# Kernel optimization log

Hardware: AMD Instinct MI355X
Metric: run time of the kernel (lower is better)

## Reference

```python
import jax, jax.numpy as jnp
import numpy as np
import math

B, H, L, D = 4, 16, 8192, 64


def setup_inputs() -> dict:
    key = jax.random.key(0)
    kq, kk, kv, kmu = jax.random.split(key, 4)
    Q = jax.random.normal(kq, (B, H, L, D), dtype=jnp.float32)
    K = jax.random.normal(kk, (B, H, L, D), dtype=jnp.float32)
    V = jax.random.normal(kv, (B, H, L, D), dtype=jnp.float32)
    mask = jnp.ones((B, L), dtype=jnp.float32)
    # learned params (multi_gauss=True): pi init [0.5,0.5]; mu ~ N(0,0.5) with mu[0]=0
    pi = jnp.array([0.5, 0.5], dtype=jnp.float32)
    mu = jax.random.normal(kmu, (2, H, D), dtype=jnp.float32) * 0.5
    mu = mu * jnp.array([0.0, 1.0], dtype=jnp.float32)[:, None, None]
    return {"Q": Q, "K": K, "V": V, "mask": mask, "pi": pi, "mu": mu}


def reference(Q, K, V, mask, pi, mu):
    # mixture-of-Gaussian keys: shift K by two learned means, convex-combine
    p = jnp.clip(pi, 0.0, 1.0)
    K1 = K - mu[0][None, :, None, :]
    K2 = K - mu[1][None, :, None, :]
    Km = K1 * p[0] + K2 * p[1]
    # kernelized linear attention: phi(x) = elu(x)+1, scaled by 1/L^0.25
    L_ = Q.shape[2]
    s = 1.0 / math.sqrt(math.sqrt(L_))
    m = mask[:, None, :, None]  # [B,1,L,1]
    Qf = (jax.nn.elu(Q) + 1.0) * s
    Kf = (jax.nn.elu(Km) + 1.0) * m * s
    Vm = V * m
    # K^T V first: [B,H,D,D] state, then Q @ state -> [B,H,L,D]
    KV = jnp.einsum('bhld,bhle->bhde', Kf, Vm)
    return jnp.einsum('bhld,bhde->bhle', Qf, KV)
```

## Files before the change

kernel.cpp:

```cpp
#include <hip/hip_runtime.h>
#include <cstddef>
#include <stdint.h>

#define L_ 8192
#define BH_ 64
#define SCALE 0.1051120519067143f
#define SLD 72

typedef __attribute__((ext_vector_type(8))) short bf16x8;
typedef __attribute__((ext_vector_type(4))) float f32x4;

__device__ __forceinline__ float elu1(float x) {
    return x > 0.0f ? (x + 1.0f) : __expf(x);
}
__device__ __forceinline__ unsigned short f2bf(float x) {
    unsigned u = __float_as_uint(x);
    u += 0x7fffu + ((u >> 16) & 1u);
    return (unsigned short)(u >> 16);
}

__global__ __launch_bounds__(256) void zero_kernel(float4* __restrict__ p) {
    p[(size_t)blockIdx.x * 256 + threadIdx.x] = make_float4(0.f, 0.f, 0.f, 0.f);
}

__global__ __launch_bounds__(256) void kv_kernel(
    const float* __restrict__ K, const float* __restrict__ V,
    const float* __restrict__ mask, const float* __restrict__ pi,
    const float* __restrict__ mu, float* __restrict__ kv)
{
    __shared__ __align__(16) unsigned short sKt[64 * SLD];
    __shared__ __align__(16) unsigned short sVt[64 * SLD];
    __shared__ float muc[64];

    const int bh = blockIdx.x;
    const int b  = bh >> 4;
    const int h  = bh & 15;
    const int l0 = blockIdx.y * 256;
    const int t    = threadIdx.x;
    const int wave = t >> 6;
    const int lane = t & 63;
    const int r = lane & 15;
    const int q = lane >> 4;

    const float p0 = fminf(fmaxf(pi[0], 0.f), 1.f);
    const float p1 = fminf(fmaxf(pi[1], 0.f), 1.f);
    const float psum = p0 + p1;
    if (t < 64) muc[t] = p0 * mu[h * 64 + t] + p1 * mu[1024 + h * 64 + t];

    const float* Kb = K + (size_t)bh * (L_ * 64);
    const float* Vb = V + (size_t)bh * (L_ * 64);
    const float* mb = mask + (size_t)b * L_;

    const int lloc = t >> 2;
    const int cb   = t & 3;

    f32x4 acc[4];
#pragma unroll
    for (int i = 0; i < 4; ++i) acc[i] = (f32x4){0.f, 0.f, 0.f, 0.f};

    __syncthreads();

#pragma unroll 1
    for (int tile = 0; tile < 4; ++tile) {
        const int lrow = l0 + tile * 64 + lloc;
        const float m = mb[lrow];
        const float sm2 = SCALE * m * m;
        const float* kp = Kb + (size_t)lrow * 64;
        const float* vp = Vb + (size_t)lrow * 64;
        if (tile) __syncthreads();
#pragma unroll
        for (int i = 0; i < 4; ++i) {
            const int c4 = cb + 4 * i;
            const float4 kk = *(const float4*)(kp + 4 * c4);
            const float4 mm = *(const float4*)(&muc[4 * c4]);
            sKt[(4 * c4 + 0) * SLD + lloc] = f2bf(elu1(kk.x * psum - mm.x) * sm2);
            sKt[(4 * c4 + 1) * SLD + lloc] = f2bf(elu1(kk.y * psum - mm.y) * sm2);
            sKt[(4 * c4 + 2) * SLD + lloc] = f2bf(elu1(kk.z * psum - mm.z) * sm2);
            sKt[(4 * c4 + 3) * SLD + lloc] = f2bf(elu1(kk.w * psum - mm.w) * sm2);
            const float4 vv = *(const float4*)(vp + 4 * c4);
            sVt[(4 * c4 + 0) * SLD + lloc] = f2bf(vv.x);
            sVt[(4 * c4 + 1) * SLD + lloc] = f2bf(vv.y);
            sVt[(4 * c4 + 2) * SLD + lloc] = f2bf(vv.z);
            sVt[(4 * c4 + 3) * SLD + lloc] = f2bf(vv.w);
        }
        __syncthreads();

        const bf16x8 a0 = *(const bf16x8*)&sKt[(16 * wave + r) * SLD + 8 * q];
        const bf16x8 a1 = *(const bf16x8*)&sKt[(16 * wave + r) * SLD + 32 + 8 * q];
#pragma unroll
        for (int nt = 0; nt < 4; ++nt) {
            const bf16x8 b0 = *(const bf16x8*)&sVt[(16 * nt + r) * SLD + 8 * q];
            const bf16x8 b1 = *(const bf16x8*)&sVt[(16 * nt + r) * SLD + 32 + 8 * q];
            acc[nt] = __builtin_amdgcn_mfma_f32_16x16x32_bf16(a0, b0, acc[nt], 0, 0, 0);
            acc[nt] = __builtin_amdgcn_mfma_f32_16x16x32_bf16(a1, b1, acc[nt], 0, 0, 0);
        }
    }

    float* kvb = kv + (size_t)bh * 4096;
#pragma unroll
    for (int nt = 0; nt < 4; ++nt)
#pragma unroll
        for (int reg = 0; reg < 4; ++reg)
            atomicAdd(kvb + (16 * wave + 4 * q + reg) * 64 + 16 * nt + r, acc[nt][reg]);
}

__global__ __launch_bounds__(256) void out_kernel(
    const float* __restrict__ Q, const float* __restrict__ kv,
    float* __restrict__ out)
{
    __shared__ __align__(16) unsigned short sKVt[64 * SLD];

    const int bh = blockIdx.x;
    const int l0 = blockIdx.y * 512;
    const int t    = threadIdx.x;
    const int wave = t >> 6;
    const int lane = t & 63;
    const int r = lane & 15;
    const int q = lane >> 4;

    {
        const float* kvb = kv + (size_t)bh * 4096 + t * 16;
        const int d  = t >> 2;
        const int e0 = (t & 3) * 16;
#pragma unroll
        for (int j4 = 0; j4 < 4; ++j4) {
            const float4 f = *(const float4*)(kvb + 4 * j4);
            sKVt[(e0 + 4 * j4 + 0) * SLD + d] = f2bf(f.x);
            sKVt[(e0 + 4 * j4 + 1) * SLD + d] = f2bf(f.y);
            sKVt[(e0 + 4 * j4 + 2) * SLD + d] = f2bf(f.z);
            sKVt[(e0 + 4 * j4 + 3) * SLD + d] = f2bf(f.w);
        }
    }
    __syncthreads();

    bf16x8 bfr[4][2];
#pragma unroll
    for (int nt = 0; nt < 4; ++nt) {
        bfr[nt][0] = *(const bf16x8*)&sKVt[(16 * nt + r) * SLD + 8 * q];
        bfr[nt][1] = *(const bf16x8*)&sKVt[(16 * nt + r) * SLD + 32 + 8 * q];
    }

    const int mbase = l0 + wave * 128;
    const float* qrow = Q + (size_t)bh * (L_ * 64) + (size_t)(mbase + r) * 64 + 8 * q;
    float* ob = out + (size_t)bh * (L_ * 64);

    float4 c0 = *(const float4*)(qrow);
    float4 c1 = *(const float4*)(qrow + 4);
    float4 c2 = *(const float4*)(qrow + 32);
    float4 c3 = *(const float4*)(qrow + 36);

#pragma unroll 1
    for (int mt = 0; mt < 8; ++mt) {
        float4 n0, n1, n2, n3;
        if (mt < 7) {
            const float* nq = qrow + (size_t)(mt + 1) * 16 * 64;
            n0 = *(const float4*)(nq);
            n1 = *(const float4*)(nq + 4);
            n2 = *(const float4*)(nq + 32);
            n3 = *(const float4*)(nq + 36);
        }
        bf16x8 a0, a1;
        a0[0] = f2bf(elu1(c0.x) * SCALE); a0[1] = f2bf(elu1(c0.y) * SCALE);
        a0[2] = f2bf(elu1(c0.z) * SCALE); a0[3] = f2bf(elu1(c0.w) * SCALE);
        a0[4] = f2bf(elu1(c1.x) * SCALE); a0[5] = f2bf(elu1(c1.y) * SCALE);
        a0[6] = f2bf(elu1(c1.z) * SCALE); a0[7] = f2bf(elu1(c1.w) * SCALE);
        a1[0] = f2bf(elu1(c2.x) * SCALE); a1[1] = f2bf(elu1(c2.y) * SCALE);
        a1[2] = f2bf(elu1(c2.z) * SCALE); a1[3] = f2bf(elu1(c2.w) * SCALE);
        a1[4] = f2bf(elu1(c3.x) * SCALE); a1[5] = f2bf(elu1(c3.y) * SCALE);
        a1[6] = f2bf(elu1(c3.z) * SCALE); a1[7] = f2bf(elu1(c3.w) * SCALE);

        f32x4 acc[4];
#pragma unroll
        for (int nt = 0; nt < 4; ++nt) {
            acc[nt] = (f32x4){0.f, 0.f, 0.f, 0.f};
            acc[nt] = __builtin_amdgcn_mfma_f32_16x16x32_bf16(a0, bfr[nt][0], acc[nt], 0, 0, 0);
            acc[nt] = __builtin_amdgcn_mfma_f32_16x16x32_bf16(a1, bfr[nt][1], acc[nt], 0, 0, 0);
        }

        float* orow = ob + (size_t)(mbase + mt * 16 + 4 * q) * 64;
#pragma unroll
        for (int nt = 0; nt < 4; ++nt)
#pragma unroll
            for (int reg = 0; reg < 4; ++reg)
                orow[(size_t)reg * 64 + 16 * nt + r] = acc[nt][reg];

        c0 = n0; c1 = n1; c2 = n2; c3 = n3;
    }
}

extern "C" void kernel_launch(void* const* d_in, const int* in_sizes, int n_in,
                              void* d_out, int out_size, void* d_ws, size_t ws_size,
                              hipStream_t stream) {
    (void)in_sizes; (void)n_in; (void)out_size; (void)ws_size;
    const float* Q    = (const float*)d_in[0];
    const float* K    = (const float*)d_in[1];
    const float* V    = (const float*)d_in[2];
    const float* mask = (const float*)d_in[3];
    const float* pi   = (const float*)d_in[4];
    const float* mu   = (const float*)d_in[5];
    float* out = (float*)d_out;
    float* kvw = (float*)d_ws;

    zero_kernel<<<256, 256, 0, stream>>>((float4*)kvw);
    kv_kernel<<<dim3(BH_, 32), 256, 0, stream>>>(K, V, mask, pi, mu, kvw);
    out_kernel<<<dim3(BH_, 16), 256, 0, stream>>>(Q, kvw, out);
}
```

Baseline: 415.9 us.

## Double-buffer KV staging, swizzle LDS, replace atomics with partial-sum reduction

The KV-state kernel now covers 512 rows per block over 16 y-blocks. It prefetches the next 64-row tile of K/V into registers while staging the current one, and ping-pongs between two LDS buffers. LDS writes are vectorized with an XOR swizzle so the transposed stores and MFMA reads avoid bank conflicts. When the workspace is large enough, the float atomics into the shared KV state are replaced by per-block partial outputs and a separate reduction kernel, which also removes the zeroing kernel. The cost is more registers and LDS per block, an extra launch, and 16MB of partial-sum traffic.

```diff
diff --git a/kernel.cpp b/kernel.cpp
--- a/kernel.cpp
+++ b/kernel.cpp
@@ -6,9 +6,11 @@
 #define BH_ 64
 #define SCALE 0.1051120519067143f
 #define SLD 72
+#define NY 16
 
 typedef __attribute__((ext_vector_type(8))) short bf16x8;
 typedef __attribute__((ext_vector_type(4))) float f32x4;
+typedef __attribute__((ext_vector_type(4))) unsigned short u16x4;
 
 __device__ __forceinline__ float elu1(float x) {
     return x > 0.0f ? (x + 1.0f) : __expf(x);
@@ -23,85 +25,136 @@
     p[(size_t)blockIdx.x * 256 + threadIdx.x] = make_float4(0.f, 0.f, 0.f, 0.f);
 }
 
-__global__ __launch_bounds__(256) void kv_kernel(
+template<bool ATOMIC>
+__global__ __launch_bounds__(256, 4) void kv_kernel2(
     const float* __restrict__ K, const float* __restrict__ V,
     const float* __restrict__ mask, const float* __restrict__ pi,
-    const float* __restrict__ mu, float* __restrict__ kv)
+    const float* __restrict__ mu, float* __restrict__ kvout)
 {
-    __shared__ __align__(16) unsigned short sKt[64 * SLD];
-    __shared__ __align__(16) unsigned short sVt[64 * SLD];
+    __shared__ __align__(16) unsigned short sKs[2][64 * SLD];
+    __shared__ __align__(16) unsigned short sVs[2][64 * SLD];
     __shared__ float muc[64];
 
     const int bh = blockIdx.x;
     const int b  = bh >> 4;
     const int h  = bh & 15;
-    const int l0 = blockIdx.y * 256;
+    const int l0 = blockIdx.y * (L_ / NY);
     const int t    = threadIdx.x;
     const int wave = t >> 6;
     const int lane = t & 63;
     const int r = lane & 15;
     const int q = lane >> 4;
+    const int dchunk = t & 15;
+    const int lquad  = t >> 4;
 
     const float p0 = fminf(fmaxf(pi[0], 0.f), 1.f);
     const float p1 = fminf(fmaxf(pi[1], 0.f), 1.f);
     const float psum = p0 + p1;
     if (t < 64) muc[t] = p0 * mu[h * 64 + t] + p1 * mu[1024 + h * 64 + t];
 
-    const float* Kb = K + (size_t)bh * (L_ * 64);
-    const float* Vb = V + (size_t)bh * (L_ * 64);
-    const float* mb = mask + (size_t)b * L_;
-
-    const int lloc = t >> 2;
-    const int cb   = t & 3;
+    const float* Kb = K + (size_t)bh * (L_ * 64) + (size_t)(l0 + 4 * lquad) * 64 + 4 * dchunk;
+    const float* Vb = V + (size_t)bh * (L_ * 64) + (size_t)(l0 + 4 * lquad) * 64 + 4 * dchunk;
+    const float* mb = mask + (size_t)b * L_ + l0 + 4 * lquad;
+
+    const int loff = (4 * lquad) ^ ((dchunk & 3) << 3);
+    const int swz  = ((r >> 2) & 3) << 3;
 
     f32x4 acc[4];
 #pragma unroll
     for (int i = 0; i < 4; ++i) acc[i] = (f32x4){0.f, 0.f, 0.f, 0.f};
 
+    f32x4 ka[4], va[4], kb_[4], vb_[4];
+    float ma_[4], mc_[4];
+
+#define KV_LOAD(tt, KR, VR, MR)                                              \
+    {                                                                        \
+        _Pragma("unroll")                                                    \
+        for (int i = 0; i < 4; ++i) {                                        \
+            KR[i] = *(const f32x4*)(Kb + (size_t)((tt) * 64 + i) * 64);      \
+            VR[i] = *(const f32x4*)(Vb + (size_t)((tt) * 64 + i) * 64);      \
+            MR[i] = mb[(tt) * 64 + i];                                       \
+        }                                                                    \
+    }
+
+#define KV_STAGE(KR, VR, MR, sKp, sVp)                                       \
+    {                                                                        \
+        const f32x4 mm = *(const f32x4*)&muc[4 * dchunk];                    \
+        float s2_[4];                                                        \
+        _Pragma("unroll")                                                    \
+        for (int i = 0; i < 4; ++i) s2_[i] = SCALE * MR[i] * MR[i];          \
+        _Pragma("unroll")                                                    \
+        for (int j = 0; j < 4; ++j) {                                        \
+            u16x4 wk, wv;                                                    \
+            _Pragma("unroll")                                                \
+            for (int i = 0; i < 4; ++i) {                                    \
+                wk[i] = f2bf(elu1(KR[i][j] * psum - mm[j]) * s2_[i]);        \
+                wv[i] = f2bf(VR[i][j]);                                      \
+            }                                                                \
+            *(u16x4*)&sKp[(4 * dchunk + j) * SLD + loff] = wk;               \
+            *(u16x4*)&sVp[(4 * dchunk + j) * SLD + loff] = wv;               \
+        }                                                                    \
+    }
+
+#define KV_MFMA(sKp, sVp)                                                    \
+    {                                                                        \
+        const int arow = (16 * wave + r) * SLD;                              \
+        const bf16x8 a0 = *(const bf16x8*)&sKp[arow + ((8 * q) ^ swz)];      \
+        const bf16x8 a1 = *(const bf16x8*)&sKp[arow + 32 + ((8 * q) ^ swz)]; \
+        _Pragma("unroll")                                                    \
+        for (int nt = 0; nt < 4; ++nt) {                                     \
+            const int brow = (16 * nt + r) * SLD;                            \
+            const bf16x8 b0 = *(const bf16x8*)&sVp[brow + ((8 * q) ^ swz)];  \
+            const bf16x8 b1 = *(const bf16x8*)&sVp[brow + 32 + ((8 * q) ^ swz)]; \
+            acc[nt] = __builtin_amdgcn_mfma_f32_16x16x32_bf16(a0, b0, acc[nt], 0, 0, 0); \
+            acc[nt] = __builtin_amdgcn_mfma_f32_16x16x32_bf16(a1, b1, acc[nt], 0, 0, 0); \
+        }                                                                    \
+    }
+
+    KV_LOAD(0, ka, va, ma_);
     __syncthreads();
 
 #pragma unroll 1
-    for (int tile = 0; tile < 4; ++tile) {
-        const int lrow = l0 + tile * 64 + lloc;
-        const float m = mb[lrow];
-        const float sm2 = SCALE * m * m;
-        const float* kp = Kb + (size_t)lrow * 64;
-        const float* vp = Vb + (size_t)lrow * 64;
-        if (tile) __syncthreads();
-#pragma unroll
-        for (int i = 0; i < 4; ++i) {
-            const int c4 = cb + 4 * i;
-            const float4 kk = *(const float4*)(kp + 4 * c4);
-            const float4 mm = *(const float4*)(&muc[4 * c4]);
-            sKt[(4 * c4 + 0) * SLD + lloc] = f2bf(elu1(kk.x * psum - mm.x) * sm2);
-            sKt[(4 * c4 + 1) * SLD + lloc] = f2bf(elu1(kk.y * psum - mm.y) * sm2);
-            sKt[(4 * c4 + 2) * SLD + lloc] = f2bf(elu1(kk.z * psum - mm.z) * sm2);
-            sKt[(4 * c4 + 3) * SLD + lloc] = f2bf(elu1(kk.w * psum - mm.w) * sm2);
-            const float4 vv = *(const float4*)(vp + 4 * c4);
-            sVt[(4 * c4 + 0) * SLD + lloc] = f2bf(vv.x);
-            sVt[(4 * c4 + 1) * SLD + lloc] = f2bf(vv.y);
-            sVt[(4 * c4 + 2) * SLD + lloc] = f2bf(vv.z);
-            sVt[(4 * c4 + 3) * SLD + lloc] = f2bf(vv.w);
-        }
+    for (int t2 = 0; t2 < 8; t2 += 2) {
+        KV_LOAD(t2 + 1, kb_, vb_, mc_);
+        KV_STAGE(ka, va, ma_, sKs[0], sVs[0]);
         __syncthreads();
-
-        const bf16x8 a0 = *(const bf16x8*)&sKt[(16 * wave + r) * SLD + 8 * q];
-        const bf16x8 a1 = *(const bf16x8*)&sKt[(16 * wave + r) * SLD + 32 + 8 * q];
-#pragma unroll
-        for (int nt = 0; nt < 4; ++nt) {
-            const bf16x8 b0 = *(const bf16x8*)&sVt[(16 * nt + r) * SLD + 8 * q];
-            const bf16x8 b1 = *(const bf16x8*)&sVt[(16 * nt + r) * SLD + 32 + 8 * q];
-            acc[nt] = __builtin_amdgcn_mfma_f32_16x16x32_bf16(a0, b0, acc[nt], 0, 0, 0);
-            acc[nt] = __builtin_amdgcn_mfma_f32_16x16x32_bf16(a1, b1, acc[nt], 0, 0, 0);
-        }
-    }
-
-    float* kvb = kv + (size_t)bh * 4096;
-#pragma unroll
-    for (int nt = 0; nt < 4; ++nt)
-#pragma unroll
-        for (int reg = 0; reg < 4; ++reg)
-            atomicAdd(kvb + (16 * wave + 4 * q + reg) * 64 + 16 * nt + r, acc[nt][reg]);
+        KV_MFMA(sKs[0], sVs[0]);
+        if (t2 + 2 < 8) { KV_LOAD(t2 + 2, ka, va, ma_); }
+        KV_STAGE(kb_, vb_, mc_, sKs[1], sVs[1]);
+        __syncthreads();
+        KV_MFMA(sKs[1], sVs[1]);
+    }
+
+    if constexpr (ATOMIC) {
+        float* kvb = kvout + (size_t)bh * 4096;
+#pragma unroll
+        for (int nt = 0; nt < 4; ++nt)
+#pragma unroll
+            for (int reg = 0; reg < 4; ++reg)
+                atomicAdd(kvb + (16 * wave + 4 * q + reg) * 64 + 16 * nt + r, acc[nt][reg]);
+    } else {
+        float* pb = kvout + ((size_t)blockIdx.y * BH_ + bh) * 4096;
+#pragma unroll
+        for (int nt = 0; nt < 4; ++nt)
+#pragma unroll
+            for (int reg = 0; reg < 4; ++reg)
+                pb[(16 * wave + 4 * q + reg) * 64 + 16 * nt + r] = acc[nt][reg];
+    }
+#undef KV_LOAD
+#undef KV_STAGE
+#undef KV_MFMA
+}
+
+__global__ __launch_bounds__(256) void reduce_kernel(
+    const float* __restrict__ pb, float* __restrict__ kv)
+{
+    const int bh = blockIdx.x;
+    const size_t idx = (size_t)blockIdx.y * 1024 + (size_t)threadIdx.x * 4;
+    f32x4 s = (f32x4){0.f, 0.f, 0.f, 0.f};
+#pragma unroll
+    for (int y = 0; y < NY; ++y)
+        s += *(const f32x4*)&pb[((size_t)y * BH_ + bh) * 4096 + idx];
+    *(f32x4*)&kv[(size_t)bh * 4096 + idx] = s;
 }
 
 __global__ __launch_bounds__(256) void out_kernel(
@@ -191,7 +244,7 @@
 extern "C" void kernel_launch(void* const* d_in, const int* in_sizes, int n_in,
                               void* d_out, int out_size, void* d_ws, size_t ws_size,
                               hipStream_t stream) {
-    (void)in_sizes; (void)n_in; (void)out_size; (void)ws_size;
+    (void)in_sizes; (void)n_in; (void)out_size;
     const float* Q    = (const float*)d_in[0];
     const float* K    = (const float*)d_in[1];
     const float* V    = (const float*)d_in[2];
@@ -199,9 +252,21 @@
     const float* pi   = (const float*)d_in[4];
     const float* mu   = (const float*)d_in[5];
     float* out = (float*)d_out;
-    float* kvw = (float*)d_ws;
-
-    zero_kernel<<<256, 256, 0, stream>>>((float4*)kvw);
-    kv_kernel<<<dim3(BH_, 32), 256, 0, stream>>>(K, V, mask, pi, mu, kvw);
-    out_kernel<<<dim3(BH_, 16), 256, 0, stream>>>(Q, kvw, out);
-}
+    float* ws  = (float*)d_ws;
+
+    const size_t part_floats = (size_t)NY * BH_ * 4096;
+    const size_t need_bytes  = (part_floats + (size_t)BH_ * 4096) * sizeof(float);
+
+    if (ws_size >= need_bytes) {
+        float* pb  = ws;
+        float* kvf = ws + part_floats;
+        kv_kernel2<false><<<dim3(BH_, NY), 256, 0, stream>>>(K, V, mask, pi, mu, pb);
+        reduce_kernel<<<dim3(BH_, 4), 256, 0, stream>>>(pb, kvf);
+        out_kernel<<<dim3(BH_, 16), 256, 0, stream>>>(Q, kvf, out);
+    } else {
+        float* kvf = ws;
+        zero_kernel<<<256, 256, 0, stream>>>((float4*)kvf);
+        kv_kernel2<true><<<dim3(BH_, NY), 256, 0, stream>>>(K, V, mask, pi, mu, kvf);
+        out_kernel<<<dim3(BH_, 16), 256, 0, stream>>>(Q, kvf, out);
+    }
+}
```

Measured after the change: 422.0 us. No clear change (+1.5%).
